# Optimization experiments

Hardware: AMD Instinct MI355X
Metric: run time of the kernel (lower is better)

## Reference

```python
import jax, jax.numpy as jnp
import numpy as np

N = 16384   # nodes
K = 10      # knn_graph(k=11) minus self-loop -> 10 neighbors per node
H = 128     # hidden_nf
L = 7       # n_layers
IN = 8      # in_node_nf
OUT = 4     # out_node_nf


def setup_inputs() -> dict:
    key = jax.random.key(0)
    ks = jax.random.split(key, 20)
    s = 0.05
    rn = lambda k, shp, sc=s: (jax.random.normal(k, shp, dtype=jnp.float32) * sc)
    return {
        "h": jax.random.normal(ks[0], (N, 3 + IN), dtype=jnp.float32) * 100.0,  # cols 0:3 coords (divided by 3330 inside), 3: features
        "idx": jax.random.randint(ks[1], (N, K), 0, N),  # neighbor (src) indices per dst node
        "emb_in_w": rn(ks[2], (IN, H)), "emb_in_b": rn(ks[3], (H,)),
        "edge_w1": rn(ks[4], (L, 2 * H + 1, H)), "edge_b1": rn(ks[5], (L, H)),
        "edge_w2": rn(ks[6], (L, H, H)), "edge_b2": rn(ks[7], (L, H)),
        "coord_w1": rn(ks[8], (L, H, H)), "coord_b1": rn(ks[9], (L, H)),
        "coord_w2": rn(ks[10], (L, H, 1), 0.001),  # xavier gain=0.001, no bias
        "node_w1": rn(ks[11], (L, 2 * H, H)), "node_b1": rn(ks[12], (L, H)),
        "node_w2": rn(ks[13], (L, H, H)), "node_b2": rn(ks[14], (L, H)),
        "emb_out_w": rn(ks[15], (H + 3, OUT)), "emb_out_b": rn(ks[16], (OUT,)),
        "step_count": 0,
    }


def reference(h, idx, emb_in_w, emb_in_b, edge_w1, edge_b1, edge_w2, edge_b2,
              coord_w1, coord_b1, coord_w2, node_w1, node_b1, node_w2, node_b2,
              emb_out_w, emb_out_b, step_count):
    silu = jax.nn.silu
    x = h[:, :3] / 3330.0                       # [N,3] coordinates
    hh = h[:, 3:] @ emb_in_w + emb_in_b         # [N,H] embedding_in (plain Linear)
    for l in range(edge_w1.shape[0]):           # 7 E_GCL layers (structurally distinct params)
        # --- RelativePositionCordMessage (per-edge, edges = (idx[i,k] -> i)) ---
        x_s = x[idx]                            # [N,K,3] src coords (gather)
        hh_s = hh[idx]                          # [N,K,H] src features (gather)
        diff = x_s - x[:, None, :]              # src - dst
        radial = jnp.sum(diff * diff, axis=-1, keepdims=True)   # [N,K,1]
        hh_d = jnp.broadcast_to(hh[:, None, :], hh_s.shape)
        ef = jnp.concatenate([radial, hh_s, hh_d], axis=-1)     # [N,K,2H+1]
        ef = silu(ef @ edge_w1[l] + edge_b1[l])
        ef = silu(ef @ edge_w2[l] + edge_b2[l])                 # edge_feature [N,K,H]
        cm = silu(ef @ coord_w1[l] + coord_b1[l]) @ coord_w2[l] # [N,K,1] (no bias, no tanh)
        trans = diff * cm                                        # [N,K,3]
        # --- Aggregationlayer (mailbox mean/sum reduce + node MLP) ---
        trans = jnp.clip(trans, -1000.0, 1000.0)
        x = jnp.clip(x, -1000.0, 1000.0) + jnp.mean(trans, axis=1)
        agg = jnp.concatenate([hh, jnp.sum(ef, axis=1)], axis=-1)  # [N,2H]
        dh = silu(agg @ node_w1[l] + node_b1[l]) @ node_w2[l] + node_b2[l]
        hh = hh + dh                                              # residual=True
    out = jnp.concatenate([hh, x], axis=-1) @ emb_out_w + emb_out_b  # embedding_out [N,4]
    return out
```

## Files before the change

kernel.cpp:

```cpp
#include <hip/hip_runtime.h>
#include <hip/hip_bf16.h>

#define NN 16384
#define KNN 10
#define HD 128
#define NL 7
#define TM 8
#define EDG 80
#define NE (NN*KNN)

#define W1E_OFF 0
#define W1D_OFF 16384
#define W2_OFF  32768
#define C1_OFF  49152
#define N1_OFF  65536
#define N2_OFF  98304
#define WL_STRIDE 114688

typedef float fv4 __attribute__((ext_vector_type(4)));
typedef short bv8 __attribute__((ext_vector_type(8)));

static __device__ __forceinline__ unsigned short f2b(float f) {
  __hip_bfloat16 h = __float2bfloat16(f);
  return __builtin_bit_cast(unsigned short, h);
}
static __device__ __forceinline__ float b2f(unsigned short u) {
  unsigned int x = ((unsigned int)u) << 16;
  return __builtin_bit_cast(float, x);
}
static __device__ __forceinline__ unsigned int pk2(float lo, float hi) {
  unsigned int r;
  asm("v_cvt_pk_bf16_f32 %0, %1, %2" : "=v"(r) : "v"(lo), "v"(hi));
  return r;
}
static __device__ __forceinline__ float silu_f(float x) {
  return x * __builtin_amdgcn_rcpf(1.0f + __expf(-x));
}
#define MFMA(a,b,c) __builtin_amdgcn_mfma_f32_16x16x32_bf16((a),(b),(c),0,0,0)

#define GLOAD_LDS(gp, lp) \
  __builtin_amdgcn_global_load_lds((const __attribute__((address_space(1))) void*)(gp), \
                                   (__attribute__((address_space(3))) void*)(lp), 16, 0, 0)

static __device__ __forceinline__ int swz8(int row, int col) {
  return row * 128 + (col ^ ((row & 7) << 3));
}

__global__ void prep_kernel(const float* __restrict__ ew1, const float* __restrict__ ew2,
                            const float* __restrict__ cw1, const float* __restrict__ nw1,
                            const float* __restrict__ nw2, unsigned short* __restrict__ wt)
{
  int g = blockIdx.x * 256 + threadIdx.x;
  if (g >= NL * WL_STRIDE) return;
  int l = g / WL_STRIDE;
  int r = g % WL_STRIDE;
  float v;
  if (r < 16384) {
    int c = r >> 7, k = r & 127;
    v = ew1[(l*257 + 1 + k)*128 + c];
  } else if (r < 32768) {
    int q = r - 16384; int c = q >> 7, k = q & 127;
    v = ew1[(l*257 + 129 + k)*128 + c];
  } else if (r < 49152) {
    int q = r - 32768; int c = q >> 7, k = q & 127;
    v = ew2[(l*128 + k)*128 + c];
  } else if (r < 65536) {
    int q = r - 49152; int c = q >> 7, k = q & 127;
    v = cw1[(l*128 + k)*128 + c];
  } else if (r < 98304) {
    int q = r - 65536; int c = q >> 8, k = q & 255;
    v = nw1[(l*256 + k)*128 + c];
  } else {
    int q = r - 98304; int c = q >> 7, k = q & 127;
    v = nw2[(l*128 + k)*128 + c];
  }
  wt[g] = f2b(v);
}

__global__ void init_kernel(const float* __restrict__ h, const float* __restrict__ eiw,
                            const float* __restrict__ eib,
                            unsigned short* __restrict__ hhb, float* __restrict__ x)
{
  int g = blockIdx.x * 256 + threadIdx.x;
  int n = g >> 7, c = g & 127;
  float acc = eib[c];
  #pragma unroll
  for (int j = 0; j < 8; ++j) acc += h[n*11 + 3 + j] * eiw[j*128 + c];
  hhb[g] = f2b(acc);
  if (c < 3) x[n*4 + c] = h[n*11 + c] * (1.0f/3330.0f);
  if (c == 3) x[n*4 + 3] = 0.f;
}

__global__ void out_kernel(const unsigned short* __restrict__ hhb, const float* __restrict__ x,
                           const float* __restrict__ ow, const float* __restrict__ ob,
                           float* __restrict__ out)
{
  __shared__ float sOW[131*4];
  int tid = threadIdx.x;
  for (int i = tid; i < 131*4; i += 256) sOW[i] = ow[i];
  __syncthreads();
  int g = blockIdx.x * 256 + tid;
  int n = g >> 2, o = g & 3;
  float acc = ob[o];
  #pragma unroll
  for (int kk = 0; kk < 16; ++kk) {
    bv8 v = *(const bv8*)(hhb + n*128 + kk*8);
    #pragma unroll
    for (int j = 0; j < 8; ++j)
      acc += b2f((unsigned short)v[j]) * sOW[(kk*8 + j)*4 + o];
  }
  #pragma unroll
  for (int d = 0; d < 3; ++d) acc += x[n*4 + d] * sOW[(128 + d)*4 + o];
  out[g] = acc;
}

static __device__ __forceinline__ void load_w8(bv8* w, const unsigned short* __restrict__ W,
                                               int cwb, int lr, int lh) {
  #pragma unroll
  for (int ks = 0; ks < 4; ++ks) {
    w[ks]     = *(const bv8*)(W + (cwb      + lr)*128 + ks*32 + lh*8);
    w[4 + ks] = *(const bv8*)(W + (cwb + 16 + lr)*128 + ks*32 + lh*8);
  }
}

__global__ __launch_bounds__(256, 3) void edge_kernel(
    const int* __restrict__ idxp,
    const unsigned short* __restrict__ wt,
    const float* __restrict__ eb1, const float* __restrict__ eb2,
    const float* __restrict__ cb1, const float* __restrict__ cw2,
    const float* __restrict__ w1r0p,
    const unsigned short* __restrict__ hhbin,
    const float* __restrict__ xin,
    unsigned short* __restrict__ aggg,
    float* __restrict__ diffg,
    float* __restrict__ cmPg)
{
  __shared__ __align__(16) unsigned char smem[40960];
  unsigned short* sA  = (unsigned short*)(smem);
  unsigned short* sB  = (unsigned short*)(smem + 20480);
  float*          sHC = (float*)(smem + 20480);
  unsigned short* sEf = sA;

  const int tid  = threadIdx.x;
  const int wave = tid >> 6;
  const int lane = tid & 63;
  const int lr   = lane & 15;
  const int lh   = lane >> 4;
  const int cwb  = wave * 32;
  const int cb0  = cwb + lh*4;
  const int node0 = blockIdx.x * TM;

  #pragma unroll
  for (int it = 0; it < 5; ++it) {
    int q = tid + it*256;
    int e = q >> 4, cq = q & 15;
    int s = idxp[node0*KNN + e];
    int csw = (cq ^ (e & 7)) << 3;
    GLOAD_LDS(hhbin + s*HD + csw, sA + ((q & ~63) << 3));
  }

  bv8 hb[4];
  #pragma unroll
  for (int ks = 0; ks < 4; ++ks)
    hb[ks] = *(const bv8*)(hhbin + (node0 + (lr & 7))*HD + ks*32 + lh*8);
  bv8 wd[8]; load_w8(wd, wt + W1D_OFF, cwb, lr, lh);
  fv4 cw2v0 = *(const fv4*)(cw2 + cb0);
  fv4 cw2v1 = *(const fv4*)(cw2 + cb0 + 16);
  fv4 w1r0v0 = *(const fv4*)(w1r0p + cb0);
  fv4 w1r0v1 = *(const fv4*)(w1r0p + cb0 + 16);

  if (tid < EDG) {
    int e = tid, n = e / KNN;
    int s = idxp[node0*KNN + e];
    fv4 xs4 = *(const fv4*)(xin + s*4);
    fv4 xd4 = *(const fv4*)(xin + (node0+n)*4);
    float d0 = xs4[0]-xd4[0], d1 = xs4[1]-xd4[1], d2 = xs4[2]-xd4[2];
    float rad = d0*d0 + d1*d1 + d2*d2;
    fv4 dv = (fv4){d0, d1, d2, rad};
    *(fv4*)(diffg + (node0*KNN + e)*4) = dv;
  }
  {
    fv4 hac0 = *(const fv4*)(eb1 + cb0);
    fv4 hac1 = *(const fv4*)(eb1 + cb0 + 16);
    #pragma unroll
    for (int ks = 0; ks < 4; ++ks) {
      hac0 = MFMA(wd[ks],   hb[ks], hac0);
      hac1 = MFMA(wd[4+ks], hb[ks], hac1);
    }
    if (lr < TM) {
      *(fv4*)(sHC + lr*132 + cb0)      = hac0;
      *(fv4*)(sHC + lr*132 + cb0 + 16) = hac1;
    }
  }
  bv8 we[8]; load_w8(we, wt + W1E_OFF, cwb, lr, lh);

  fv4 acc[5][2];
  #pragma unroll
  for (int n = 0; n < 5; ++n) {
    int e = n*16 + lr;
    int nd = e / KNN;
    int s = idxp[node0*KNN + e];
    fv4 xs4 = *(const fv4*)(xin + s*4);
    fv4 xd4 = *(const fv4*)(xin + (node0+nd)*4);
    float d0 = xs4[0]-xd4[0], d1 = xs4[1]-xd4[1], d2 = xs4[2]-xd4[2];
    float rad = d0*d0 + d1*d1 + d2*d2;
    fv4 h0 = *(const fv4*)(sHC + nd*132 + cb0);
    fv4 h1 = *(const fv4*)(sHC + nd*132 + cb0 + 16);
    acc[n][0] = h0 + w1r0v0*rad;
    acc[n][1] = h1 + w1r0v1*rad;
  }
  fv4 e2b0 = *(const fv4*)(eb2 + cb0);
  fv4 e2b1 = *(const fv4*)(eb2 + cb0 + 16);
  __syncthreads();

  bv8 w2r[8]; load_w8(w2r, wt + W2_OFF, cwb, lr, lh);
  {
    __builtin_amdgcn_s_setprio(1);
    #pragma unroll
    for (int ks = 0; ks < 4; ++ks) {
      #pragma unroll
      for (int n = 0; n < 5; ++n) {
        bv8 b = *(const bv8*)(sA + swz8(n*16 + lr, ks*32 + lh*8));
        acc[n][0] = MFMA(we[ks],   b, acc[n][0]);
        acc[n][1] = MFMA(we[4+ks], b, acc[n][1]);
      }
    }
    __builtin_amdgcn_s_setprio(0);
    #pragma unroll
    for (int n = 0; n < 5; ++n) {
      int e = n*16 + lr;
      #pragma unroll
      for (int mt = 0; mt < 2; ++mt) {
        uint2 p;
        p.x = pk2(silu_f(acc[n][mt][0]), silu_f(acc[n][mt][1]));
        p.y = pk2(silu_f(acc[n][mt][2]), silu_f(acc[n][mt][3]));
        *(uint2*)(sB + swz8(e, cb0 + mt*16)) = p;
      }
    }
  }
  __syncthreads();

  bv8 c1r[8]; load_w8(c1r, wt + C1_OFF, cwb, lr, lh);
  fv4 c1b0 = *(const fv4*)(cb1 + cb0);
  fv4 c1b1 = *(const fv4*)(cb1 + cb0 + 16);
  {
    fv4 acc2[5][2];
    #pragma unroll
    for (int n = 0; n < 5; ++n) { acc2[n][0] = e2b0; acc2[n][1] = e2b1; }
    __builtin_amdgcn_s_setprio(1);
    #pragma unroll
    for (int ks = 0; ks < 4; ++ks) {
      #pragma unroll
      for (int n = 0; n < 5; ++n) {
        bv8 b = *(const bv8*)(sB + swz8(n*16 + lr, ks*32 + lh*8));
        acc2[n][0] = MFMA(w2r[ks],   b, acc2[n][0]);
        acc2[n][1] = MFMA(w2r[4+ks], b, acc2[n][1]);
      }
    }
    __builtin_amdgcn_s_setprio(0);
    #pragma unroll
    for (int n = 0; n < 5; ++n) {
      int e = n*16 + lr;
      #pragma unroll
      for (int mt = 0; mt < 2; ++mt) {
        uint2 p;
        p.x = pk2(silu_f(acc2[n][mt][0]), silu_f(acc2[n][mt][1]));
        p.y = pk2(silu_f(acc2[n][mt][2]), silu_f(acc2[n][mt][3]));
        *(uint2*)(sA + swz8(e, cb0 + mt*16)) = p;
      }
    }
  }
  __syncthreads();

  {
    fv4 acc3[5][2];
    #pragma unroll
    for (int n = 0; n < 5; ++n) { acc3[n][0] = c1b0; acc3[n][1] = c1b1; }
    __builtin_amdgcn_s_setprio(1);
    #pragma unroll
    for (int ks = 0; ks < 4; ++ks) {
      #pragma unroll
      for (int n = 0; n < 5; ++n) {
        bv8 b = *(const bv8*)(sEf + swz8(n*16 + lr, ks*32 + lh*8));
        acc3[n][0] = MFMA(c1r[ks],   b, acc3[n][0]);
        acc3[n][1] = MFMA(c1r[4+ks], b, acc3[n][1]);
      }
    }
    __builtin_amdgcn_s_setprio(0);
    #pragma unroll
    for (int n = 0; n < 5; ++n) {
      float pm = 0.f;
      #pragma unroll
      for (int j = 0; j < 4; ++j) {
        pm += silu_f(acc3[n][0][j]) * cw2v0[j];
        pm += silu_f(acc3[n][1][j]) * cw2v1[j];
      }
      pm += __shfl_xor(pm, 16);
      pm += __shfl_xor(pm, 32);
      if (lane < 16) cmPg[wave*NE + node0*KNN + n*16 + lr] = pm;
    }
    if (tid >= 128) {
      int q = tid - 128;
      int n = q >> 4, c = (q & 15) << 3;
      float s[8] = {0,0,0,0,0,0,0,0};
      #pragma unroll
      for (int k = 0; k < KNN; ++k) {
        bv8 v = *(const bv8*)(sEf + swz8(n*KNN + k, c));
        #pragma unroll
        for (int e8 = 0; e8 < 8; ++e8) s[e8] += b2f((unsigned short)v[e8]);
      }
      uint4 pv = make_uint4(pk2(s[0], s[1]), pk2(s[2], s[3]),
                            pk2(s[4], s[5]), pk2(s[6], s[7]));
      *(uint4*)(aggg + (node0 + n)*HD + c) = pv;
    }
  }
}

__global__ __launch_bounds__(256, 3) void node_kernel(
    const unsigned short* __restrict__ wt,
    const float* __restrict__ nb1, const float* __restrict__ nb2,
    const unsigned short* __restrict__ hhbin,
    const unsigned short* __restrict__ aggg,
    const float* __restrict__ diffg,
    const float* __restrict__ cmPg,
    const float* __restrict__ xin, float* __restrict__ xout,
    unsigned short* __restrict__ hhbout)
{
  __shared__ __align__(16) unsigned char smem[49152];
  unsigned short* sIn0 = (unsigned short*)(smem);
  unsigned short* sIn1 = (unsigned short*)(smem + 16384);
  unsigned short* sN1  = (unsigned short*)(smem + 32768);

  const int tid  = threadIdx.x;
  const int lane = tid & 63;
  const int wave = tid >> 6;
  const int lr   = lane & 15;
  const int lh   = lane >> 4;
  const int cwb  = wave * 32;
  const int cb0  = cwb + lh*4;
  const int node0 = blockIdx.x * 64;

  #pragma unroll
  for (int it = 0; it < 4; ++it) {
    int q = tid + it*256;
    int r = q >> 4, cq = q & 15;
    int csw = (cq ^ (r & 7)) << 3;
    GLOAD_LDS(hhbin + (node0 + r)*HD + csw, sIn0 + ((q & ~63) << 3));
  }
  #pragma unroll
  for (int it = 0; it < 4; ++it) {
    int q = tid + it*256;
    int r = q >> 4, cq = q & 15;
    int csw = (cq ^ (r & 7)) << 3;
    GLOAD_LDS(aggg + (node0 + r)*HD + csw, sIn1 + ((q & ~63) << 3));
  }
  bv8 n1r[16];
  #pragma unroll
  for (int ks = 0; ks < 8; ++ks) {
    n1r[ks]     = *(const bv8*)(wt + N1_OFF + (cwb      + lr)*256 + ks*32 + lh*8);
    n1r[8 + ks] = *(const bv8*)(wt + N1_OFF + (cwb + 16 + lr)*256 + ks*32 + lh*8);
  }
  if (tid < 192) {
    int n = tid / 3, d = tid % 3;
    int e0 = (node0 + n)*KNN;
    float xo = xin[(node0+n)*4 + d];
    xo = fminf(fmaxf(xo, -1000.f), 1000.f);
    float s = 0.f;
    #pragma unroll
    for (int k = 0; k < KNN; ++k) {
      int e = e0 + k;
      float cm = cmPg[e] + cmPg[NE + e] + cmPg[2*NE + e] + cmPg[3*NE + e];
      float tr = diffg[e*4 + d] * cm;
      tr = fminf(fmaxf(tr, -1000.f), 1000.f);
      s += tr;
    }
    xout[(node0+n)*4 + d] = xo + s * (1.0f/KNN);
  }
  __syncthreads();

  {
    fv4 bb0 = *(const fv4*)(nb1 + cb0);
    fv4 bb1 = *(const fv4*)(nb1 + cb0 + 16);
    #pragma unroll
    for (int t = 0; t < 4; ++t) {
      fv4 acc0 = bb0, acc1 = bb1;
      #pragma unroll
      for (int ks = 0; ks < 4; ++ks) {
        bv8 b0 = *(const bv8*)(sIn0 + swz8(t*16 + lr, ks*32 + lh*8));
        bv8 b1 = *(const bv8*)(sIn1 + swz8(t*16 + lr, ks*32 + lh*8));
        acc0 = MFMA(n1r[ks],      b0, acc0);
        acc0 = MFMA(n1r[4+ks],    b1, acc0);
        acc1 = MFMA(n1r[8+ks],    b0, acc1);
        acc1 = MFMA(n1r[12+ks],   b1, acc1);
      }
      uint2 p0, p1;
      p0.x = pk2(silu_f(acc0[0]), silu_f(acc0[1]));
      p0.y = pk2(silu_f(acc0[2]), silu_f(acc0[3]));
      p1.x = pk2(silu_f(acc1[0]), silu_f(acc1[1]));
      p1.y = pk2(silu_f(acc1[2]), silu_f(acc1[3]));
      *(uint2*)(sN1 + swz8(t*16 + lr, cb0))      = p0;
      *(uint2*)(sN1 + swz8(t*16 + lr, cb0 + 16)) = p1;
    }
  }
  __syncthreads();

  {
    bv8 n2r[8]; load_w8(n2r, wt + N2_OFF, cwb, lr, lh);
    fv4 bb0 = *(const fv4*)(nb2 + cb0);
    fv4 bb1 = *(const fv4*)(nb2 + cb0 + 16);
    #pragma unroll
    for (int t = 0; t < 4; ++t) {
      fv4 acc0 = bb0, acc1 = bb1;
      #pragma unroll
      for (int ks = 0; ks < 4; ++ks) {
        bv8 b = *(const bv8*)(sN1 + swz8(t*16 + lr, ks*32 + lh*8));
        acc0 = MFMA(n2r[ks],   b, acc0);
        acc1 = MFMA(n2r[4+ks], b, acc1);
      }
      uint2 r0 = *(const uint2*)(sIn0 + swz8(t*16 + lr, cb0));
      uint2 r1 = *(const uint2*)(sIn0 + swz8(t*16 + lr, cb0 + 16));
      float v0 = b2f((unsigned short)(r0.x))       + acc0[0];
      float v1 = b2f((unsigned short)(r0.x >> 16)) + acc0[1];
      float v2 = b2f((unsigned short)(r0.y))       + acc0[2];
      float v3 = b2f((unsigned short)(r0.y >> 16)) + acc0[3];
      float w0 = b2f((unsigned short)(r1.x))       + acc1[0];
      float w1 = b2f((unsigned short)(r1.x >> 16)) + acc1[1];
      float w2 = b2f((unsigned short)(r1.y))       + acc1[2];
      float w3 = b2f((unsigned short)(r1.y >> 16)) + acc1[3];
      int g = (node0 + t*16 + lr)*HD + cb0;
      uint2 p;
      p.x = pk2(v0, v1); p.y = pk2(v2, v3);
      *(uint2*)(hhbout + g) = p;
      p.x = pk2(w0, w1); p.y = pk2(w2, w3);
      *(uint2*)(hhbout + g + 16) = p;
    }
  }
}

extern "C" void kernel_launch(void* const* d_in, const int* in_sizes, int n_in,
                              void* d_out, int out_size, void* d_ws, size_t ws_size,
                              hipStream_t stream)
{
  (void)in_sizes; (void)n_in; (void)out_size; (void)ws_size;
  const float* h   = (const float*)d_in[0];
  const int*   idx = (const int*)d_in[1];
  const float* eiw = (const float*)d_in[2];
  const float* eib = (const float*)d_in[3];
  const float* ew1 = (const float*)d_in[4];
  const float* eb1 = (const float*)d_in[5];
  const float* ew2 = (const float*)d_in[6];
  const float* eb2 = (const float*)d_in[7];
  const float* cw1 = (const float*)d_in[8];
  const float* cb1 = (const float*)d_in[9];
  const float* cw2 = (const float*)d_in[10];
  const float* nw1 = (const float*)d_in[11];
  const float* nb1 = (const float*)d_in[12];
  const float* nw2 = (const float*)d_in[13];
  const float* nb2 = (const float*)d_in[14];
  const float* eow = (const float*)d_in[15];
  const float* eob = (const float*)d_in[16];

  unsigned char* ws = (unsigned char*)d_ws;
  unsigned short* wt    = (unsigned short*)ws;
  unsigned short* hhbA  = (unsigned short*)(ws + 1605632);
  unsigned short* hhbB  = (unsigned short*)(ws + 5799936);
  float*          xA    = (float*)(ws + 9994240);
  float*          xB    = (float*)(ws + 10256384);
  unsigned short* aggg  = (unsigned short*)(ws + 10518528);
  float*          diffg = (float*)(ws + 14712832);
  float*          cmPg  = (float*)(ws + 17334272);

  prep_kernel<<<(NL*WL_STRIDE + 255)/256, 256, 0, stream>>>(ew1, ew2, cw1, nw1, nw2, wt);
  init_kernel<<<NN*HD/256, 256, 0, stream>>>(h, eiw, eib, hhbA, xA);

  unsigned short* hbs = hhbA; unsigned short* hbd = hhbB;
  float* xs = xA; float* xd = xB;
  for (int l = 0; l < NL; ++l) {
    edge_kernel<<<NN/TM, 256, 0, stream>>>(idx, wt + (size_t)l*WL_STRIDE,
        eb1 + l*128, eb2 + l*128, cb1 + l*128, cw2 + l*128,
        ew1 + (size_t)l*257*128,
        hbs, xs, aggg, diffg, cmPg);
    node_kernel<<<NN/64, 256, 0, stream>>>(wt + (size_t)l*WL_STRIDE,
        nb1 + l*128, nb2 + l*128,
        hbs, aggg, diffg, cmPg, xs, xd, hbd);
    unsigned short* ht = hbs; hbs = hbd; hbd = ht;
    float* t = xs; xs = xd; xd = t;
  }
  out_kernel<<<NN*4/256, 256, 0, stream>>>(hbs, xs, eow, eob, (float*)d_out);
}
```

Measured before the change: 438.9 us.

## Process four edge tiles per block with double-buffered gather prefetch

After: 762.6 us. 73.7% more time.

```diff
diff --git a/kernel.cpp b/kernel.cpp
--- a/kernel.cpp
+++ b/kernel.cpp
@@ -8,6 +8,7 @@
 #define TM 8
 #define EDG 80
 #define NE (NN*KNN)
+#define TPB 4
 
 #define W1E_OFF 0
 #define W1D_OFF 16384
@@ -123,6 +124,54 @@
   }
 }
 
+static __device__ __forceinline__ void stage_tile(
+    const int* __restrict__ idxp, const unsigned short* __restrict__ hhbin,
+    const float* __restrict__ xin, float* __restrict__ diffg,
+    unsigned short* __restrict__ dstbuf, float* __restrict__ sRad,
+    int node0t, int tid)
+{
+  #pragma unroll
+  for (int it = 0; it < 5; ++it) {
+    int q = tid + it*256;
+    int e = q >> 4, cq = q & 15;
+    int s = idxp[node0t*KNN + e];
+    int csw = (cq ^ (e & 7)) << 3;
+    GLOAD_LDS(hhbin + s*HD + csw, dstbuf + ((q & ~63) << 3));
+  }
+  if (tid < EDG) {
+    int e = tid, n = e / KNN;
+    int s = idxp[node0t*KNN + e];
+    fv4 xs4 = *(const fv4*)(xin + s*4);
+    fv4 xd4 = *(const fv4*)(xin + (node0t+n)*4);
+    float d0 = xs4[0]-xd4[0], d1 = xs4[1]-xd4[1], d2 = xs4[2]-xd4[2];
+    float rad = d0*d0 + d1*d1 + d2*d2;
+    sRad[e] = rad;
+    fv4 dv = (fv4){d0, d1, d2, rad};
+    *(fv4*)(diffg + (node0t*KNN + e)*4) = dv;
+  }
+}
+
+static __device__ __forceinline__ void hc_tile(
+    const unsigned short* __restrict__ hhbin, const bv8* wd,
+    fv4 hcb0, fv4 hcb1, float* __restrict__ sHC,
+    int node0t, int lr, int lh, int cb0)
+{
+  bv8 hb[4];
+  #pragma unroll
+  for (int ks = 0; ks < 4; ++ks)
+    hb[ks] = *(const bv8*)(hhbin + (node0t + (lr & 7))*HD + ks*32 + lh*8);
+  fv4 hac0 = hcb0, hac1 = hcb1;
+  #pragma unroll
+  for (int ks = 0; ks < 4; ++ks) {
+    hac0 = MFMA(wd[ks],   hb[ks], hac0);
+    hac1 = MFMA(wd[4+ks], hb[ks], hac1);
+  }
+  if (lr < TM) {
+    *(fv4*)(sHC + lr*132 + cb0)      = hac0;
+    *(fv4*)(sHC + lr*132 + cb0 + 16) = hac1;
+  }
+}
+
 __global__ __launch_bounds__(256, 3) void edge_kernel(
     const int* __restrict__ idxp,
     const unsigned short* __restrict__ wt,
@@ -135,11 +184,11 @@
     float* __restrict__ diffg,
     float* __restrict__ cmPg)
 {
-  __shared__ __align__(16) unsigned char smem[40960];
-  unsigned short* sA  = (unsigned short*)(smem);
-  unsigned short* sB  = (unsigned short*)(smem + 20480);
-  float*          sHC = (float*)(smem + 20480);
-  unsigned short* sEf = sA;
+  __shared__ __align__(16) unsigned char smem[45504];
+  unsigned short* bufA = (unsigned short*)(smem);
+  unsigned short* bufB = (unsigned short*)(smem + 20480);
+  float*          sHC  = (float*)(smem + 40960);
+  float*          sRad = (float*)(smem + 45184);
 
   const int tid  = threadIdx.x;
   const int wave = tid >> 6;
@@ -148,171 +197,148 @@
   const int lh   = lane >> 4;
   const int cwb  = wave * 32;
   const int cb0  = cwb + lh*4;
-  const int node0 = blockIdx.x * TM;
-
-  #pragma unroll
-  for (int it = 0; it < 5; ++it) {
-    int q = tid + it*256;
-    int e = q >> 4, cq = q & 15;
-    int s = idxp[node0*KNN + e];
-    int csw = (cq ^ (e & 7)) << 3;
-    GLOAD_LDS(hhbin + s*HD + csw, sA + ((q & ~63) << 3));
-  }
-
-  bv8 hb[4];
-  #pragma unroll
-  for (int ks = 0; ks < 4; ++ks)
-    hb[ks] = *(const bv8*)(hhbin + (node0 + (lr & 7))*HD + ks*32 + lh*8);
+  const int node0 = blockIdx.x * (TM * TPB);
+
   bv8 wd[8]; load_w8(wd, wt + W1D_OFF, cwb, lr, lh);
   fv4 cw2v0 = *(const fv4*)(cw2 + cb0);
   fv4 cw2v1 = *(const fv4*)(cw2 + cb0 + 16);
   fv4 w1r0v0 = *(const fv4*)(w1r0p + cb0);
   fv4 w1r0v1 = *(const fv4*)(w1r0p + cb0 + 16);
-
-  if (tid < EDG) {
-    int e = tid, n = e / KNN;
-    int s = idxp[node0*KNN + e];
-    fv4 xs4 = *(const fv4*)(xin + s*4);
-    fv4 xd4 = *(const fv4*)(xin + (node0+n)*4);
-    float d0 = xs4[0]-xd4[0], d1 = xs4[1]-xd4[1], d2 = xs4[2]-xd4[2];
-    float rad = d0*d0 + d1*d1 + d2*d2;
-    fv4 dv = (fv4){d0, d1, d2, rad};
-    *(fv4*)(diffg + (node0*KNN + e)*4) = dv;
-  }
-  {
-    fv4 hac0 = *(const fv4*)(eb1 + cb0);
-    fv4 hac1 = *(const fv4*)(eb1 + cb0 + 16);
-    #pragma unroll
-    for (int ks = 0; ks < 4; ++ks) {
-      hac0 = MFMA(wd[ks],   hb[ks], hac0);
-      hac1 = MFMA(wd[4+ks], hb[ks], hac1);
+  fv4 hcb0 = *(const fv4*)(eb1 + cb0);
+  fv4 hcb1 = *(const fv4*)(eb1 + cb0 + 16);
+
+  stage_tile(idxp, hhbin, xin, diffg, bufA, sRad, node0, tid);
+  hc_tile(hhbin, wd, hcb0, hcb1, sHC, node0, lr, lh, cb0);
+  bv8 we[8]; load_w8(we, wt + W1E_OFF, cwb, lr, lh);
+  __syncthreads();
+
+  unsigned short* G = bufA;
+  unsigned short* O = bufB;
+
+  for (int t = 0; t < TPB; ++t) {
+    const int node0t = node0 + t*TM;
+
+    bv8 w2r[8]; load_w8(w2r, wt + W2_OFF, cwb, lr, lh);
+    {
+      fv4 acc[5][2];
+      #pragma unroll
+      for (int n = 0; n < 5; ++n) {
+        int e = n*16 + lr;
+        int nd = e / KNN;
+        float rad = sRad[e];
+        fv4 h0 = *(const fv4*)(sHC + nd*132 + cb0);
+        fv4 h1 = *(const fv4*)(sHC + nd*132 + cb0 + 16);
+        acc[n][0] = h0 + w1r0v0*rad;
+        acc[n][1] = h1 + w1r0v1*rad;
+      }
+      __builtin_amdgcn_s_setprio(1);
+      #pragma unroll
+      for (int ks = 0; ks < 4; ++ks) {
+        #pragma unroll
+        for (int n = 0; n < 5; ++n) {
+          bv8 b = *(const bv8*)(G + swz8(n*16 + lr, ks*32 + lh*8));
+          acc[n][0] = MFMA(we[ks],   b, acc[n][0]);
+          acc[n][1] = MFMA(we[4+ks], b, acc[n][1]);
+        }
+      }
+      __builtin_amdgcn_s_setprio(0);
+      #pragma unroll
+      for (int n = 0; n < 5; ++n) {
+        int e = n*16 + lr;
+        #pragma unroll
+        for (int mt = 0; mt < 2; ++mt) {
+          uint2 p;
+          p.x = pk2(silu_f(acc[n][mt][0]), silu_f(acc[n][mt][1]));
+          p.y = pk2(silu_f(acc[n][mt][2]), silu_f(acc[n][mt][3]));
+          *(uint2*)(O + swz8(e, cb0 + mt*16)) = p;
+        }
+      }
     }
-    if (lr < TM) {
-      *(fv4*)(sHC + lr*132 + cb0)      = hac0;
-      *(fv4*)(sHC + lr*132 + cb0 + 16) = hac1;
+    __syncthreads();
+
+    bv8 c1r[8]; load_w8(c1r, wt + C1_OFF, cwb, lr, lh);
+    {
+      fv4 bb0 = *(const fv4*)(eb2 + cb0);
+      fv4 bb1 = *(const fv4*)(eb2 + cb0 + 16);
+      fv4 acc2[5][2];
+      #pragma unroll
+      for (int n = 0; n < 5; ++n) { acc2[n][0] = bb0; acc2[n][1] = bb1; }
+      __builtin_amdgcn_s_setprio(1);
+      #pragma unroll
+      for (int ks = 0; ks < 4; ++ks) {
+        #pragma unroll
+        for (int n = 0; n < 5; ++n) {
+          bv8 b = *(const bv8*)(O + swz8(n*16 + lr, ks*32 + lh*8));
+          acc2[n][0] = MFMA(w2r[ks],   b, acc2[n][0]);
+          acc2[n][1] = MFMA(w2r[4+ks], b, acc2[n][1]);
+        }
+      }
+      __builtin_amdgcn_s_setprio(0);
+      #pragma unroll
+      for (int n = 0; n < 5; ++n) {
+        int e = n*16 + lr;
+        #pragma unroll
+        for (int mt = 0; mt < 2; ++mt) {
+          uint2 p;
+          p.x = pk2(silu_f(acc2[n][mt][0]), silu_f(acc2[n][mt][1]));
+          p.y = pk2(silu_f(acc2[n][mt][2]), silu_f(acc2[n][mt][3]));
+          *(uint2*)(G + swz8(e, cb0 + mt*16)) = p;
+        }
+      }
     }
-  }
-  bv8 we[8]; load_w8(we, wt + W1E_OFF, cwb, lr, lh);
-
-  fv4 acc[5][2];
-  #pragma unroll
-  for (int n = 0; n < 5; ++n) {
-    int e = n*16 + lr;
-    int nd = e / KNN;
-    int s = idxp[node0*KNN + e];
-    fv4 xs4 = *(const fv4*)(xin + s*4);
-    fv4 xd4 = *(const fv4*)(xin + (node0+nd)*4);
-    float d0 = xs4[0]-xd4[0], d1 = xs4[1]-xd4[1], d2 = xs4[2]-xd4[2];
-    float rad = d0*d0 + d1*d1 + d2*d2;
-    fv4 h0 = *(const fv4*)(sHC + nd*132 + cb0);
-    fv4 h1 = *(const fv4*)(sHC + nd*132 + cb0 + 16);
-    acc[n][0] = h0 + w1r0v0*rad;
-    acc[n][1] = h1 + w1r0v1*rad;
-  }
-  fv4 e2b0 = *(const fv4*)(eb2 + cb0);
-  fv4 e2b1 = *(const fv4*)(eb2 + cb0 + 16);
-  __syncthreads();
-
-  bv8 w2r[8]; load_w8(w2r, wt + W2_OFF, cwb, lr, lh);
-  {
-    __builtin_amdgcn_s_setprio(1);
-    #pragma unroll
-    for (int ks = 0; ks < 4; ++ks) {
+    __syncthreads();
+
+    if (t + 1 < TPB)
+      stage_tile(idxp, hhbin, xin, diffg, O, sRad, node0t + TM, tid);
+    {
+      fv4 bb0 = *(const fv4*)(cb1 + cb0);
+      fv4 bb1 = *(const fv4*)(cb1 + cb0 + 16);
+      fv4 acc3[5][2];
+      #pragma unroll
+      for (int n = 0; n < 5; ++n) { acc3[n][0] = bb0; acc3[n][1] = bb1; }
+      __builtin_amdgcn_s_setprio(1);
+      #pragma unroll
+      for (int ks = 0; ks < 4; ++ks) {
+        #pragma unroll
+        for (int n = 0; n < 5; ++n) {
+          bv8 b = *(const bv8*)(G + swz8(n*16 + lr, ks*32 + lh*8));
+          acc3[n][0] = MFMA(c1r[ks],   b, acc3[n][0]);
+          acc3[n][1] = MFMA(c1r[4+ks], b, acc3[n][1]);
+        }
+      }
+      __builtin_amdgcn_s_setprio(0);
       #pragma unroll
       for (int n = 0; n < 5; ++n) {
-        bv8 b = *(const bv8*)(sA + swz8(n*16 + lr, ks*32 + lh*8));
-        acc[n][0] = MFMA(we[ks],   b, acc[n][0]);
-        acc[n][1] = MFMA(we[4+ks], b, acc[n][1]);
-      }
+        float pm = 0.f;
+        #pragma unroll
+        for (int j = 0; j < 4; ++j) {
+          pm += silu_f(acc3[n][0][j]) * cw2v0[j];
+          pm += silu_f(acc3[n][1][j]) * cw2v1[j];
+        }
+        pm += __shfl_xor(pm, 16);
+        pm += __shfl_xor(pm, 32);
+        if (lane < 16) cmPg[wave*NE + node0t*KNN + n*16 + lr] = pm;
+      }
+      if (tid >= 128) {
+        int q = tid - 128;
+        int n = q >> 4, c = (q & 15) << 3;
+        float s[8] = {0,0,0,0,0,0,0,0};
+        #pragma unroll
+        for (int k = 0; k < KNN; ++k) {
+          bv8 v = *(const bv8*)(G + swz8(n*KNN + k, c));
+          #pragma unroll
+          for (int e8 = 0; e8 < 8; ++e8) s[e8] += b2f((unsigned short)v[e8]);
+        }
+        uint4 pv = make_uint4(pk2(s[0], s[1]), pk2(s[2], s[3]),
+                              pk2(s[4], s[5]), pk2(s[6], s[7]));
+        *(uint4*)(aggg + (node0t + n)*HD + c) = pv;
+      }
+      if (t + 1 < TPB)
+        hc_tile(hhbin, wd, hcb0, hcb1, sHC, node0t + TM, lr, lh, cb0);
     }
-    __builtin_amdgcn_s_setprio(0);
-    #pragma unroll
-    for (int n = 0; n < 5; ++n) {
-      int e = n*16 + lr;
-      #pragma unroll
-      for (int mt = 0; mt < 2; ++mt) {
-        uint2 p;
-        p.x = pk2(silu_f(acc[n][mt][0]), silu_f(acc[n][mt][1]));
-        p.y = pk2(silu_f(acc[n][mt][2]), silu_f(acc[n][mt][3]));
-        *(uint2*)(sB + swz8(e, cb0 + mt*16)) = p;
-      }
-    }
-  }
-  __syncthreads();
-
-  bv8 c1r[8]; load_w8(c1r, wt + C1_OFF, cwb, lr, lh);
-  fv4 c1b0 = *(const fv4*)(cb1 + cb0);
-  fv4 c1b1 = *(const fv4*)(cb1 + cb0 + 16);
-  {
-    fv4 acc2[5][2];
-    #pragma unroll
-    for (int n = 0; n < 5; ++n) { acc2[n][0] = e2b0; acc2[n][1] = e2b1; }
-    __builtin_amdgcn_s_setprio(1);
-    #pragma unroll
-    for (int ks = 0; ks < 4; ++ks) {
-      #pragma unroll
-      for (int n = 0; n < 5; ++n) {
-        bv8 b = *(const bv8*)(sB + swz8(n*16 + lr, ks*32 + lh*8));
-        acc2[n][0] = MFMA(w2r[ks],   b, acc2[n][0]);
-        acc2[n][1] = MFMA(w2r[4+ks], b, acc2[n][1]);
-      }
-    }
-    __builtin_amdgcn_s_setprio(0);
-    #pragma unroll
-    for (int n = 0; n < 5; ++n) {
-      int e = n*16 + lr;
-      #pragma unroll
-      for (int mt = 0; mt < 2; ++mt) {
-        uint2 p;
-        p.x = pk2(silu_f(acc2[n][mt][0]), silu_f(acc2[n][mt][1]));
-        p.y = pk2(silu_f(acc2[n][mt][2]), silu_f(acc2[n][mt][3]));
-        *(uint2*)(sA + swz8(e, cb0 + mt*16)) = p;
-      }
-    }
-  }
-  __syncthreads();
-
-  {
-    fv4 acc3[5][2];
-    #pragma unroll
-    for (int n = 0; n < 5; ++n) { acc3[n][0] = c1b0; acc3[n][1] = c1b1; }
-    __builtin_amdgcn_s_setprio(1);
-    #pragma unroll
-    for (int ks = 0; ks < 4; ++ks) {
-      #pragma unroll
-      for (int n = 0; n < 5; ++n) {
-        bv8 b = *(const bv8*)(sEf + swz8(n*16 + lr, ks*32 + lh*8));
-        acc3[n][0] = MFMA(c1r[ks],   b, acc3[n][0]);
-        acc3[n][1] = MFMA(c1r[4+ks], b, acc3[n][1]);
-      }
-    }
-    __builtin_amdgcn_s_setprio(0);
-    #pragma unroll
-    for (int n = 0; n < 5; ++n) {
-      float pm = 0.f;
-      #pragma unroll
-      for (int j = 0; j < 4; ++j) {
-        pm += silu_f(acc3[n][0][j]) * cw2v0[j];
-        pm += silu_f(acc3[n][1][j]) * cw2v1[j];
-      }
-      pm += __shfl_xor(pm, 16);
-      pm += __shfl_xor(pm, 32);
-      if (lane < 16) cmPg[wave*NE + node0*KNN + n*16 + lr] = pm;
-    }
-    if (tid >= 128) {
-      int q = tid - 128;
-      int n = q >> 4, c = (q & 15) << 3;
-      float s[8] = {0,0,0,0,0,0,0,0};
-      #pragma unroll
-      for (int k = 0; k < KNN; ++k) {
-        bv8 v = *(const bv8*)(sEf + swz8(n*KNN + k, c));
-        #pragma unroll
-        for (int e8 = 0; e8 < 8; ++e8) s[e8] += b2f((unsigned short)v[e8]);
-      }
-      uint4 pv = make_uint4(pk2(s[0], s[1]), pk2(s[2], s[3]),
-                            pk2(s[4], s[5]), pk2(s[6], s[7]));
-      *(uint4*)(aggg + (node0 + n)*HD + c) = pv;
-    }
+    __syncthreads();
+
+    unsigned short* tmp = G; G = O; O = tmp;
   }
 }
 
@@ -476,7 +502,7 @@
   unsigned short* hbs = hhbA; unsigned short* hbd = hhbB;
   float* xs = xA; float* xd = xB;
   for (int l = 0; l < NL; ++l) {
-    edge_kernel<<<NN/TM, 256, 0, stream>>>(idx, wt + (size_t)l*WL_STRIDE,
+    edge_kernel<<<NN/(TM*TPB), 256, 0, stream>>>(idx, wt + (size_t)l*WL_STRIDE,
         eb1 + l*128, eb2 + l*128, cb1 + l*128, cw2 + l*128,
         ew1 + (size_t)l*257*128,
         hbs, xs, aggg, diffg, cmPg);
```
